# Kernel optimization log

Measured on AMD Instinct MI355X. Metric: run time of the kernel, lower is better.

Reference implementation:

```python
import jax, jax.numpy as jnp
import numpy as np

N_NODES = 100000
N_EDGES = 1600000
IN_DIM = 128
EMB_DIM = 32
K_HOPS = 3


def setup_inputs() -> dict:
    key = jax.random.key(0)
    k1, k2, k3, k4, k5, k6 = jax.random.split(key, 6)
    x = jax.random.normal(k1, (N_NODES, IN_DIM), dtype=jnp.float32)
    W = jax.random.normal(k2, (EMB_DIM, IN_DIM), dtype=jnp.float32) * (1.0 / np.sqrt(IN_DIM))
    b = jax.random.normal(k3, (EMB_DIM,), dtype=jnp.float32) * 0.01
    w = jax.random.uniform(k4, (N_EDGES,), dtype=jnp.float32)
    src = jax.random.randint(k5, (N_EDGES,), 0, N_NODES, dtype=jnp.int64)
    dst = jax.random.randint(k6, (N_EDGES,), 0, N_NODES, dtype=jnp.int64)
    return {"x": x, "W": W, "b": b, "w": w, "src": src, "dst": dst, "k": K_HOPS}


def reference(x, W, b, w, src, dst, k):
    # x: [N, in_dim] -> relu(linear) -> [N, emb_dim]
    h = jax.nn.relu(jnp.einsum("ni,ei->ne", x, W) + b)
    n_nodes = x.shape[0]
    # k hops of edge-weighted gather-multiply-scatter (u_mul_e / sum)
    for _ in range(k):
        msg = h[src] * w[:, None]              # [E, emb_dim]
        h = jax.ops.segment_sum(msg, dst, num_segments=n_nodes)
    return h
```

## Files before the change

kernel.cpp:

```cpp
#include <hip/hip_runtime.h>

constexpr int N_NODES_C = 100000;
constexpr int N_EDGES_C = 1600000;
constexpr int IN_DIM_C  = 128;
constexpr int EMB       = 32;

constexpr int NPB   = 64;
constexpr int NB    = (N_NODES_C + NPB - 1) / NPB;
constexpr int NCOL  = 8;
constexpr int NCNT  = NB * NCOL;
constexpr int SCAN_PER = (NCNT + 255) / 256;

__global__ __launch_bounds__(256) void linear_relu_kernel(
    const float* __restrict__ x, const float* __restrict__ W,
    const float* __restrict__ b, float* __restrict__ h, int n)
{
    int row = blockIdx.x * 256 + threadIdx.x;
    if (row >= n) return;
    const float4* __restrict__ xr =
        reinterpret_cast<const float4*>(x + (size_t)row * IN_DIM_C);
    const float4* __restrict__ W4 = reinterpret_cast<const float4*>(W);

    float acc[EMB];
#pragma unroll
    for (int e = 0; e < EMB; ++e) acc[e] = 0.f;

#pragma unroll 2
    for (int k4 = 0; k4 < IN_DIM_C / 4; ++k4) {
        float4 xv = xr[k4];
#pragma unroll
        for (int e = 0; e < EMB; ++e) {
            float4 wv = W4[e * (IN_DIM_C / 4) + k4];
            acc[e] = fmaf(xv.x, wv.x,
                     fmaf(xv.y, wv.y,
                     fmaf(xv.z, wv.z,
                     fmaf(xv.w, wv.w, acc[e]))));
        }
    }

    float* __restrict__ out = h + (size_t)row * EMB;
#pragma unroll
    for (int e = 0; e < EMB; ++e) {
        float v = acc[e] + b[e];
        out[e] = v > 0.f ? v : 0.f;
    }
}

__global__ __launch_bounds__(256) void hist8_kernel(
    const int* __restrict__ dst, int* __restrict__ cnt8)
{
    int e = blockIdx.x * 256 + threadIdx.x;
    if (e < N_EDGES_C)
        atomicAdd(&cnt8[(dst[e] >> 6) * NCOL + (blockIdx.x & 7)], 1);
}

__global__ __launch_bounds__(256) void scan12k_kernel(
    const int* __restrict__ cnt8, int* __restrict__ boff8, int* __restrict__ cur8)
{
    int t = threadIdx.x;
    int base = t * SCAN_PER;
    int v[SCAN_PER];
    int s = 0;
#pragma unroll
    for (int i = 0; i < SCAN_PER; ++i) {
        int x = (base + i < NCNT) ? cnt8[base + i] : 0;
        v[i] = x; s += x;
    }
    int lane = t & 63, wid = t >> 6;
    int inc = s;
#pragma unroll
    for (int o = 1; o < 64; o <<= 1) {
        int u = __shfl_up(inc, o, 64);
        if (lane >= o) inc += u;
    }
    __shared__ int wtot[4];
    if (lane == 63) wtot[wid] = inc;
    __syncthreads();
    int wbase = 0;
    for (int i = 0; i < wid; ++i) wbase += wtot[i];
    int run = wbase + inc - s;
#pragma unroll
    for (int i = 0; i < SCAN_PER; ++i) {
        if (base + i < NCNT) { boff8[base + i] = run; cur8[base + i] = 0; }
        run += v[i];
    }
    if (t == 255) boff8[NCNT] = run;
}

__global__ __launch_bounds__(256) void cfill_kernel(
    const int* __restrict__ src, const int* __restrict__ dst,
    const float* __restrict__ w, const int* __restrict__ boff8,
    int* __restrict__ cur8, int2* __restrict__ recs)
{
    int e = blockIdx.x * 256 + threadIdx.x;
    if (e >= N_EDGES_C) return;
    int d   = dst[e];
    int idx = (d >> 6) * NCOL + (blockIdx.x & 7);
    int pos = boff8[idx] + atomicAdd(&cur8[idx], 1);
    recs[pos] = make_int2(src[e] | ((d & 63) << 17), __float_as_int(w[e]));
}

__global__ __launch_bounds__(256) void sort_kernel(
    const int2* __restrict__ recs, const int* __restrict__ boff8,
    int2* __restrict__ recs2, int* __restrict__ nodeoff)
{
    __shared__ int hist[NPB];
    __shared__ int pfx[NPB];
    __shared__ int cur[NPB];
    int t = threadIdx.x;
    int b = blockIdx.x;
    if (t < NPB) { hist[t] = 0; cur[t] = 0; }
    __syncthreads();

    int beg = boff8[b * NCOL];
    int end = boff8[(b + 1) * NCOL];

    for (int j = beg + t; j < end; j += 256)
        atomicAdd(&hist[(recs[j].x >> 17) & 63], 1);
    __syncthreads();

    if (t == 0) {
        int run = 0;
        for (int i = 0; i < NPB; ++i) { pfx[i] = run; run += hist[i]; }
    }
    __syncthreads();

    if (t < NPB) {
        int node = b * NPB + t;
        if (node <= N_NODES_C) nodeoff[node] = beg + pfx[t];
    }

    for (int j = beg + t; j < end; j += 256) {
        int2 r = recs[j];
        int dlow = (r.x >> 17) & 63;
        int pos  = beg + pfx[dlow] + atomicAdd(&cur[dlow], 1);
        recs2[pos] = make_int2(r.x & 0x1FFFF, r.y);
    }
}

__global__ __launch_bounds__(256) void hop_csr_kernel(
    const float* __restrict__ h_in, const int* __restrict__ nodeoff,
    const int2* __restrict__ recs2, float* __restrict__ h_out)
{
    int tid = blockIdx.x * 256 + threadIdx.x;
    int node = tid >> 3;
    int q    = tid & 7;
    if (node >= N_NODES_C) return;

    int beg = nodeoff[node], end = nodeoff[node + 1];
    float4 acc = make_float4(0.f, 0.f, 0.f, 0.f);
    int j = beg;
    for (; j + 4 <= end; j += 4) {
        int2 ep0 = recs2[j + 0];
        int2 ep1 = recs2[j + 1];
        int2 ep2 = recs2[j + 2];
        int2 ep3 = recs2[j + 3];
        float4 h0 = *reinterpret_cast<const float4*>(h_in + (size_t)ep0.x * EMB + q * 4);
        float4 h1 = *reinterpret_cast<const float4*>(h_in + (size_t)ep1.x * EMB + q * 4);
        float4 h2 = *reinterpret_cast<const float4*>(h_in + (size_t)ep2.x * EMB + q * 4);
        float4 h3 = *reinterpret_cast<const float4*>(h_in + (size_t)ep3.x * EMB + q * 4);
        float w0 = __int_as_float(ep0.y), w1 = __int_as_float(ep1.y);
        float w2 = __int_as_float(ep2.y), w3 = __int_as_float(ep3.y);
        acc.x = fmaf(h0.x, w0, acc.x); acc.y = fmaf(h0.y, w0, acc.y);
        acc.z = fmaf(h0.z, w0, acc.z); acc.w = fmaf(h0.w, w0, acc.w);
        acc.x = fmaf(h1.x, w1, acc.x); acc.y = fmaf(h1.y, w1, acc.y);
        acc.z = fmaf(h1.z, w1, acc.z); acc.w = fmaf(h1.w, w1, acc.w);
        acc.x = fmaf(h2.x, w2, acc.x); acc.y = fmaf(h2.y, w2, acc.y);
        acc.z = fmaf(h2.z, w2, acc.z); acc.w = fmaf(h2.w, w2, acc.w);
        acc.x = fmaf(h3.x, w3, acc.x); acc.y = fmaf(h3.y, w3, acc.y);
        acc.z = fmaf(h3.z, w3, acc.z); acc.w = fmaf(h3.w, w3, acc.w);
    }
    for (; j < end; ++j) {
        int2  ep = recs2[j];
        float wt = __int_as_float(ep.y);
        float4 hv = *reinterpret_cast<const float4*>(h_in + (size_t)ep.x * EMB + q * 4);
        acc.x = fmaf(hv.x, wt, acc.x);
        acc.y = fmaf(hv.y, wt, acc.y);
        acc.z = fmaf(hv.z, wt, acc.z);
        acc.w = fmaf(hv.w, wt, acc.w);
    }
    *reinterpret_cast<float4*>(h_out + (size_t)node * EMB + q * 4) = acc;
}

extern "C" void kernel_launch(void* const* d_in, const int* in_sizes, int n_in,
                              void* d_out, int out_size, void* d_ws, size_t ws_size,
                              hipStream_t stream) {
    const float* x   = (const float*)d_in[0];
    const float* W   = (const float*)d_in[1];
    const float* b   = (const float*)d_in[2];
    const float* w   = (const float*)d_in[3];
    const int*   src = (const int*)d_in[4];
    const int*   dst = (const int*)d_in[5];

    float* out = (float*)d_out;

    char* ws = (char*)d_ws;
    size_t o = 0;
    auto alloc = [&](size_t bytes) {
        char* p = ws + o;
        o += (bytes + 255) & ~(size_t)255;
        return p;
    };
    float* h0      = (float*)alloc((size_t)N_NODES_C * EMB * sizeof(float));
    int*   cnt8    = (int*)  alloc((size_t)NCNT * sizeof(int));
    int*   boff8   = (int*)  alloc((size_t)(NCNT + 1) * sizeof(int));
    int*   cur8    = (int*)  alloc((size_t)NCNT * sizeof(int));
    int*   nodeoff = (int*)  alloc((size_t)(N_NODES_C + 1) * sizeof(int));
    int2*  recs    = (int2*) alloc((size_t)N_EDGES_C * sizeof(int2));
    int2*  recs2   = (int2*) alloc((size_t)N_EDGES_C * sizeof(int2));

    const int EB = (N_EDGES_C + 255) / 256;
    const int HB = (N_NODES_C * 8 + 255) / 256;

    hipMemsetAsync(cnt8, 0, (size_t)NCNT * sizeof(int), stream);
    hist8_kernel<<<EB, 256, 0, stream>>>(dst, cnt8);
    scan12k_kernel<<<1, 256, 0, stream>>>(cnt8, boff8, cur8);
    cfill_kernel<<<EB, 256, 0, stream>>>(src, dst, w, boff8, cur8, recs);
    sort_kernel<<<NB, 256, 0, stream>>>(recs, boff8, recs2, nodeoff);

    linear_relu_kernel<<<(N_NODES_C + 255) / 256, 256, 0, stream>>>(
        x, W, b, h0, N_NODES_C);

    hop_csr_kernel<<<HB, 256, 0, stream>>>(h0, nodeoff, recs2, out);
    hop_csr_kernel<<<HB, 256, 0, stream>>>(out, nodeoff, recs2, h0);
    hop_csr_kernel<<<HB, 256, 0, stream>>>(h0, nodeoff, recs2, out);
}
```

Baseline: 439.1 us.

## Stage x tiles in LDS for linear layer and use nontemporal edge loads

The linear+ReLU kernel now loads a 64-row tile of x into padded shared memory with coalesced float4 loads. Each wave then computes 8 output columns for 64 rows, with the W index uniform across the wave. The old version had each thread stride through its own 512-byte row, giving uncoalesced reads, and held 32 accumulators. The cfill kernel also reads src/dst/w with nontemporal loads to avoid polluting the cache. The cost is LDS traffic and smaller per-thread work, and the gain is limited to the linear stage, which is a modest share of the total time.

```diff
diff --git a/kernel.cpp b/kernel.cpp
--- a/kernel.cpp
+++ b/kernel.cpp
@@ -11,38 +11,62 @@
 constexpr int NCNT  = NB * NCOL;
 constexpr int SCAN_PER = (NCNT + 255) / 256;
 
-__global__ __launch_bounds__(256) void linear_relu_kernel(
+constexpr int RPB = 64;
+constexpr int XS  = 129;
+
+__global__ __launch_bounds__(256) void linear_relu_lds_kernel(
     const float* __restrict__ x, const float* __restrict__ W,
-    const float* __restrict__ b, float* __restrict__ h, int n)
-{
-    int row = blockIdx.x * 256 + threadIdx.x;
-    if (row >= n) return;
-    const float4* __restrict__ xr =
-        reinterpret_cast<const float4*>(x + (size_t)row * IN_DIM_C);
+    const float* __restrict__ b, float* __restrict__ h)
+{
+    __shared__ float xs[RPB * XS];
+    int t = threadIdx.x;
+    int rbase = blockIdx.x * RPB;
+
+#pragma unroll
+    for (int i = 0; i < 8; ++i) {
+        int f  = t + i * 256;
+        int r  = f >> 5;
+        int c4 = f & 31;
+        int row = rbase + r;
+        float4 v = make_float4(0.f, 0.f, 0.f, 0.f);
+        if (row < N_NODES_C)
+            v = *reinterpret_cast<const float4*>(
+                    x + (size_t)row * IN_DIM_C + c4 * 4);
+        float* p = &xs[r * XS + c4 * 4];
+        p[0] = v.x; p[1] = v.y; p[2] = v.z; p[3] = v.w;
+    }
+    __syncthreads();
+
+    int lane = t & 63;
+    int e0   = __builtin_amdgcn_readfirstlane((t >> 6) * 8);
+    int row  = rbase + lane;
+
+    float acc[8];
+#pragma unroll
+    for (int j = 0; j < 8; ++j) acc[j] = 0.f;
+
     const float4* __restrict__ W4 = reinterpret_cast<const float4*>(W);
-
-    float acc[EMB];
-#pragma unroll
-    for (int e = 0; e < EMB; ++e) acc[e] = 0.f;
-
-#pragma unroll 2
+#pragma unroll 4
     for (int k4 = 0; k4 < IN_DIM_C / 4; ++k4) {
-        float4 xv = xr[k4];
-#pragma unroll
-        for (int e = 0; e < EMB; ++e) {
-            float4 wv = W4[e * (IN_DIM_C / 4) + k4];
-            acc[e] = fmaf(xv.x, wv.x,
-                     fmaf(xv.y, wv.y,
-                     fmaf(xv.z, wv.z,
-                     fmaf(xv.w, wv.w, acc[e]))));
+        const float* xr = &xs[lane * XS + k4 * 4];
+        float xv0 = xr[0], xv1 = xr[1], xv2 = xr[2], xv3 = xr[3];
+#pragma unroll
+        for (int j = 0; j < 8; ++j) {
+            float4 wv = W4[(e0 + j) * (IN_DIM_C / 4) + k4];
+            acc[j] = fmaf(xv0, wv.x,
+                     fmaf(xv1, wv.y,
+                     fmaf(xv2, wv.z,
+                     fmaf(xv3, wv.w, acc[j]))));
         }
     }
 
-    float* __restrict__ out = h + (size_t)row * EMB;
-#pragma unroll
-    for (int e = 0; e < EMB; ++e) {
-        float v = acc[e] + b[e];
-        out[e] = v > 0.f ? v : 0.f;
+    if (row < N_NODES_C) {
+        float* outp = h + (size_t)row * EMB + e0;
+#pragma unroll
+        for (int j = 0; j < 8; ++j) {
+            float v = acc[j] + b[e0 + j];
+            outp[j] = v > 0.f ? v : 0.f;
+        }
     }
 }
 
@@ -94,10 +118,12 @@
 {
     int e = blockIdx.x * 256 + threadIdx.x;
     if (e >= N_EDGES_C) return;
-    int d   = dst[e];
+    int   d  = __builtin_nontemporal_load(&dst[e]);
+    int   s  = __builtin_nontemporal_load(&src[e]);
+    float wt = __builtin_nontemporal_load(&w[e]);
     int idx = (d >> 6) * NCOL + (blockIdx.x & 7);
     int pos = boff8[idx] + atomicAdd(&cur8[idx], 1);
-    recs[pos] = make_int2(src[e] | ((d & 63) << 17), __float_as_int(w[e]));
+    recs[pos] = make_int2(s | ((d & 63) << 17), __float_as_int(wt));
 }
 
 __global__ __launch_bounds__(256) void sort_kernel(
@@ -211,6 +237,7 @@
 
     const int EB = (N_EDGES_C + 255) / 256;
     const int HB = (N_NODES_C * 8 + 255) / 256;
+    const int LB = (N_NODES_C + RPB - 1) / RPB;
 
     hipMemsetAsync(cnt8, 0, (size_t)NCNT * sizeof(int), stream);
     hist8_kernel<<<EB, 256, 0, stream>>>(dst, cnt8);
@@ -218,8 +245,7 @@
     cfill_kernel<<<EB, 256, 0, stream>>>(src, dst, w, boff8, cur8, recs);
     sort_kernel<<<NB, 256, 0, stream>>>(recs, boff8, recs2, nodeoff);
 
-    linear_relu_kernel<<<(N_NODES_C + 255) / 256, 256, 0, stream>>>(
-        x, W, b, h0, N_NODES_C);
+    linear_relu_lds_kernel<<<LB, 256, 0, stream>>>(x, W, b, h0);
 
     hop_csr_kernel<<<HB, 256, 0, stream>>>(h0, nodeoff, recs2, out);
     hop_csr_kernel<<<HB, 256, 0, stream>>>(out, nodeoff, recs2, h0);
```

Result: faster. 413.7 us (-5.8%).
